# Kernel optimization log

Measured on AMD Instinct MI355X. Metric: run time of the kernel, lower is better.

Reference implementation:

```python
import jax, jax.numpy as jnp
import numpy as np

N, K, M, F = 131072, 32, 65536, 64  # queries, neighbors, table rows, alpha channels


def setup_inputs() -> dict:
    key = jax.random.key(0)
    k1, k2, k3 = jax.random.split(key, 3)
    d = jax.random.uniform(k1, (N, K), dtype=jnp.float32)          # squared knn distances
    i = jax.random.randint(k2, (N, K), 0, M)                        # knn indices into alpha
    alpha = jax.random.normal(k3, (M, F), dtype=jnp.float32)        # learned coefficients
    sigma = jnp.ones((1,), dtype=jnp.float32)                       # kernel lengthscale
    return {"d": d, "i": i, "alpha": alpha, "sigma": sigma}


def reference(d, i, alpha, sigma):
    # torch: sum(alpha_[i].permute(2,0,1) * exp(-0.5*d/sigma**2), dim=2) -> [F, N]
    w = jnp.exp(-0.5 * d / (sigma[0] ** 2))          # [N, K] Gaussian weights
    gathered = jnp.take(alpha, i, axis=0)            # [N, K, F] irregular gather
    return jnp.einsum('nkf,nk->fn', gathered, w)     # weighted sum over neighbors -> [F, N]
```

## Files before the change

kernel.cpp:

```cpp
#include <hip/hip_runtime.h>
#include <hip/hip_fp16.h>


#define N_Q    131072
#define K_NB   32
#define F_CH   64
#define M_ROWS 65536

__global__ __launch_bounds__(256) void cvt_alpha_f16(
    const float* __restrict__ alpha, __half* __restrict__ a16)
{
    const int t = blockIdx.x * 256 + threadIdx.x;
    const float4 v0 = ((const float4*)alpha)[(size_t)t * 2 + 0];
    const float4 v1 = ((const float4*)alpha)[(size_t)t * 2 + 1];
    union { __half2 h2[4]; uint4 u; } pk;
    pk.h2[0] = __floats2half2_rn(v0.x, v0.y);
    pk.h2[1] = __floats2half2_rn(v0.z, v0.w);
    pk.h2[2] = __floats2half2_rn(v1.x, v1.y);
    pk.h2[3] = __floats2half2_rn(v1.z, v1.w);
    ((uint4*)a16)[t] = pk.u;
}

__global__ __launch_bounds__(512) void knn_exp_mix(
    const float*  __restrict__ dmat,
    const int*    __restrict__ imat,
    const __half* __restrict__ a16,
    const float*  __restrict__ sigma,
    float*        __restrict__ out)
{
    __shared__ float    tile[64][65];
    __shared__ unsigned sortbuf[8][8][32];

    const int lane = threadIdx.x & 63;
    const int wave = threadIdx.x >> 6;
    const int n0   = blockIdx.x * 64;
    const bool hi  = (lane >= 32);

    const float s = sigma[0];
    const float c = -0.5f / (s * s);

    const int nbase = n0 + wave * 8;
    const char* pbase = hi
        ? (const char*)&imat[(size_t)nbase * K_NB + (lane - 32)]
        : (const char*)&dmat[(size_t)nbase * K_NB + lane];
    unsigned raw[8];
    #pragma unroll
    for (int qi = 0; qi < 8; ++qi)
        raw[qi] = __builtin_nontemporal_load(
            (const unsigned*)(pbase + (size_t)qi * (K_NB * 4)));

    __builtin_amdgcn_sched_barrier(0);

    #pragma unroll
    for (int qi = 0; qi < 8; ++qi) {
        const float wv = __expf(c * __uint_as_float(raw[qi]));
        const int   iv = (int)raw[qi];

        const unsigned hbits = (unsigned)__half_as_ushort(__float2half_rn(wv));
        const unsigned hb    = (unsigned)__shfl((int)hbits, lane & 31);

        const int quart = (iv >> 14) & 3;
        const unsigned long long m0 = __ballot(hi && quart == 0);
        const unsigned long long m1 = __ballot(hi && quart == 1);
        const unsigned long long m2 = __ballot(hi && quart == 2);
        const unsigned long long m3 = __ballot(hi && quart == 3);
        const int b1 = __popcll(m0);
        const int b2 = b1 + __popcll(m1);
        const int b3 = b2 + __popcll(m2);
        const unsigned long long mq =
            (quart == 0) ? m0 : (quart == 1) ? m1 : (quart == 2) ? m2 : m3;
        const int bq =
            (quart == 0) ? 0 : (quart == 1) ? b1 : (quart == 2) ? b2 : b3;
        const unsigned long long below = (1ull << lane) - 1ull;
        const int pos = bq + __popcll(mq & below);

        if (hi)
            sortbuf[wave][qi][pos] = ((unsigned)iv << 16) | (hb & 0xFFFFu);
    }

    unsigned pv[8];
    float    acc[8];
    #pragma unroll
    for (int qi = 0; qi < 8; ++qi) {
        pv[qi]  = sortbuf[wave][qi][lane & 31];
        acc[qi] = 0.0f;
    }

    #pragma unroll
    for (int p = 0; p < 4; ++p) {
        #pragma unroll
        for (int qi = 0; qi < 8; ++qi) {
            #pragma unroll
            for (int j = 0; j < 8; ++j) {
                const int pk = __builtin_amdgcn_readlane(
                    (int)pv[qi], p * 8 + j);
                const unsigned off = (((unsigned)pk) >> 16) << 7;
                const unsigned short* addr =
                    (const unsigned short*)((const char*)a16 + off) + lane;
                const unsigned uq = (unsigned)*addr;
                asm("v_fma_mix_f32 %0, %1, %2, %0 op_sel:[0,0,0] op_sel_hi:[1,1,0]"
                    : "+v"(acc[qi])
                    : "s"(pk), "v"(uq));
            }
        }
    }

    #pragma unroll
    for (int qi = 0; qi < 8; ++qi)
        tile[wave * 8 + qi][lane] = acc[qi];

    __syncthreads();

    #pragma unroll
    for (int fi = 0; fi < 8; ++fi) {
        const int f = wave * 8 + fi;
        __builtin_nontemporal_store(tile[lane][f],
                                    &out[(size_t)f * N_Q + n0 + lane]);
    }
}

__global__ __launch_bounds__(256) void knn_exp_f32(
    const float* __restrict__ dmat,
    const int*   __restrict__ imat,
    const float* __restrict__ alpha,
    const float* __restrict__ sigma,
    float*       __restrict__ out)
{
    __shared__ float tile[64][65];
    const int lane = threadIdx.x & 63;
    const int wave = threadIdx.x >> 6;
    const int n0   = blockIdx.x * 64;
    const float s = sigma[0];
    const float c = -0.5f / (s * s);

    for (int qi = 0; qi < 16; ++qi) {
        const int q = wave * 16 + qi;
        const int n = n0 + q;
        float wv = 0.0f;
        int   iv = 0;
        if (lane < 32) {
            wv = __expf(c * dmat[(size_t)n * K_NB + lane]);
        } else {
            iv = imat[(size_t)n * K_NB + (lane - 32)];
        }
        float acc = 0.0f;
        #pragma unroll
        for (int k = 0; k < K_NB; ++k) {
            const float wk = __int_as_float(
                __builtin_amdgcn_readlane(__float_as_int(wv), k));
            const int   ik = __builtin_amdgcn_readlane(iv, 32 + k);
            acc = fmaf(wk, alpha[(size_t)ik * F_CH + lane], acc);
        }
        tile[q][lane] = acc;
    }
    __syncthreads();
    #pragma unroll
    for (int fi = 0; fi < 16; ++fi) {
        const int f = wave * 16 + fi;
        out[(size_t)f * N_Q + n0 + lane] = tile[lane][f];
    }
}

extern "C" void kernel_launch(void* const* d_in, const int* in_sizes, int n_in,
                              void* d_out, int out_size, void* d_ws, size_t ws_size,
                              hipStream_t stream) {
    const float* dmat  = (const float*)d_in[0];
    const int*   imat  = (const int*)d_in[1];
    const float* alpha = (const float*)d_in[2];
    const float* sigma = (const float*)d_in[3];
    float* out = (float*)d_out;

    const size_t bytes_a16 = (size_t)M_ROWS * F_CH * sizeof(__half);

    if (ws_size >= bytes_a16) {
        __half* a16 = (__half*)d_ws;
        hipLaunchKernelGGL(cvt_alpha_f16, dim3(M_ROWS * F_CH / 8 / 256),
                           dim3(256), 0, stream, alpha, a16);
        hipLaunchKernelGGL(knn_exp_mix, dim3(N_Q / 64), dim3(512), 0,
                           stream, dmat, imat, a16, sigma, out);
    } else {
        hipLaunchKernelGGL(knn_exp_f32, dim3(N_Q / 64), dim3(256), 0, stream,
                           dmat, imat, alpha, sigma, out);
    }
}
```

Baseline: 67.05 us.

## Gather two neighbor rows per wave with 4-byte half2 loads and cross-half reduction

Each wave now splits into two 32-lane halves that process different neighbors at once. Each lane loads a 4-byte pair of fp16 channels instead of a single 2-byte value. Two fma_mix instructions accumulate the low and high channels, and a shfl_xor across the halves combines the partial sums before the LDS transpose. This halves the number of gather instructions and replaces scalar readlane broadcasts with LDS reads of the packed index/weight. The cost is more VGPRs, an extra cross-lane reduction, and a sched_barrier per query that may limit overlap.

Result: faster. 54.56 us (-18.6%).

```diff
diff --git a/kernel.cpp b/kernel.cpp
--- a/kernel.cpp
+++ b/kernel.cpp
@@ -21,7 +21,7 @@
     ((uint4*)a16)[t] = pk.u;
 }
 
-__global__ __launch_bounds__(512) void knn_exp_mix(
+__global__ __launch_bounds__(512) void knn_exp_row2(
     const float*  __restrict__ dmat,
     const int*    __restrict__ imat,
     const __half* __restrict__ a16,
@@ -35,6 +35,9 @@
     const int wave = threadIdx.x >> 6;
     const int n0   = blockIdx.x * 64;
     const bool hi  = (lane >= 32);
+    const int  h   = lane >> 5;
+    const int  l31 = lane & 31;
+    const unsigned chan_off = (unsigned)l31 * 4u;
 
     const float s = sigma[0];
     const float c = -0.5f / (s * s);
@@ -78,36 +81,37 @@
             sortbuf[wave][qi][pos] = ((unsigned)iv << 16) | (hb & 0xFFFFu);
     }
 
-    unsigned pv[8];
-    float    acc[8];
+    float accL[8], accH[8];
     #pragma unroll
-    for (int qi = 0; qi < 8; ++qi) {
-        pv[qi]  = sortbuf[wave][qi][lane & 31];
-        acc[qi] = 0.0f;
-    }
+    for (int qi = 0; qi < 8; ++qi) { accL[qi] = 0.0f; accH[qi] = 0.0f; }
 
     #pragma unroll
     for (int p = 0; p < 4; ++p) {
         #pragma unroll
         for (int qi = 0; qi < 8; ++qi) {
             #pragma unroll
-            for (int j = 0; j < 8; ++j) {
-                const int pk = __builtin_amdgcn_readlane(
-                    (int)pv[qi], p * 8 + j);
-                const unsigned off = (((unsigned)pk) >> 16) << 7;
-                const unsigned short* addr =
-                    (const unsigned short*)((const char*)a16 + off) + lane;
-                const unsigned uq = (unsigned)*addr;
+            for (int t = 0; t < 4; ++t) {
+                const unsigned e = sortbuf[wave][qi][p * 8 + t * 2 + h];
+                const unsigned off = ((e >> 16) << 7) + chan_off;
+                const unsigned dat = *(const unsigned*)((const char*)a16 + off);
                 asm("v_fma_mix_f32 %0, %1, %2, %0 op_sel:[0,0,0] op_sel_hi:[1,1,0]"
-                    : "+v"(acc[qi])
-                    : "s"(pk), "v"(uq));
+                    : "+v"(accL[qi]) : "v"(e), "v"(dat));
+                asm("v_fma_mix_f32 %0, %1, %2, %0 op_sel:[0,1,0] op_sel_hi:[1,1,0]"
+                    : "+v"(accH[qi]) : "v"(e), "v"(dat));
             }
+            __builtin_amdgcn_sched_barrier(0);
         }
     }
 
     #pragma unroll
-    for (int qi = 0; qi < 8; ++qi)
-        tile[wave * 8 + qi][lane] = acc[qi];
+    for (int qi = 0; qi < 8; ++qi) {
+        const float sL = accL[qi] + __shfl_xor(accL[qi], 32);
+        const float sH = accH[qi] + __shfl_xor(accH[qi], 32);
+        if (!hi) {
+            tile[wave * 8 + qi][2 * l31]     = sL;
+            tile[wave * 8 + qi][2 * l31 + 1] = sH;
+        }
+    }
 
     __syncthreads();
 
@@ -176,7 +180,7 @@
         __half* a16 = (__half*)d_ws;
         hipLaunchKernelGGL(cvt_alpha_f16, dim3(M_ROWS * F_CH / 8 / 256),
                            dim3(256), 0, stream, alpha, a16);
-        hipLaunchKernelGGL(knn_exp_mix, dim3(N_Q / 64), dim3(512), 0,
+        hipLaunchKernelGGL(knn_exp_row2, dim3(N_Q / 64), dim3(512), 0,
                            stream, dmat, imat, a16, sigma, out);
     } else {
         hipLaunchKernelGGL(knn_exp_f32, dim3(N_Q / 64), dim3(256), 0, stream,
```
